# Kernel tuning notes

Measured on AMD Instinct MI355X. Metric: run time of the kernel, lower is better.

Reference implementation:

```python
import jax, jax.numpy as jnp
import numpy as np

N, NUM_TOKENS, TOKEN_DIM = 32768, 8192, 768
K = 4  # hard-coded top-k in the torch forward


def setup_inputs() -> dict:
    key = jax.random.key(0)
    k1, k2 = jax.random.split(key)
    inputs_flatten = jax.random.normal(k1, (N, TOKEN_DIM), dtype=jnp.float32)
    embed = jax.random.normal(k2, (NUM_TOKENS, TOKEN_DIM), dtype=jnp.float32)  # codebook buffer
    return {"inputs_flatten": inputs_flatten, "embed": embed}


def reference(inputs_flatten, embed):
    # squared euclidean distances: [N, num_tokens]
    distances = (
        jnp.sum(inputs_flatten ** 2, axis=1, keepdims=True)
        + jnp.sum(embed ** 2, axis=1)
        - 2.0 * (inputs_flatten @ embed.T)
    )

    # k smallest distances via top_k on negated distances
    neg_vals, topk_indices = jax.lax.top_k(-distances, K)
    topk_values = -neg_vals  # ascending smallest-k distances, [N, 4]

    # drop nearest, reweight the next 3 neighbors
    tv = topk_values[:, 1:]  # [N, 3]
    tv = tv / jnp.maximum(jnp.linalg.norm(tv, axis=1, keepdims=True), 1e-12)  # F.normalize
    tv = 1.0 / (tv + 1e-4)
    topk_values = jax.nn.softmax(tv, axis=1)
    topk_indices_out = topk_indices[:, 1:]

    # hard assignment (argmin) and codebook lookup (one-hot scatter + matmul == gather)
    encoding_indices = jnp.argmin(distances, axis=1)[:, None]  # [N, 1]
    quantize = embed[encoding_indices[:, 0]]  # [N, token_dim]

    # straight-through estimator
    quantize = jax.lax.stop_gradient(quantize - inputs_flatten) + inputs_flatten
    return quantize, encoding_indices, topk_values, topk_indices_out
```

## Files before the change

### kernel.cpp

```cpp
#include <hip/hip_runtime.h>
#include <cfloat>
#include <cmath>

#define NROWS 32768
#define NTOK  8192
#define DIM   768
#define KSPLIT 384

#define BM 64
#define BN 128
#define BK 32
#define NT 512

#define Q_OFF   0
#define EI_OFF  (NROWS*DIM)
#define TV_OFF  (EI_OFF + NROWS)
#define TI_OFF  (TV_OFF + NROWS*3)

typedef short short8 __attribute__((ext_vector_type(8)));
typedef float f32x4 __attribute__((ext_vector_type(4)));
typedef float f32x16 __attribute__((ext_vector_type(16)));

__global__ __launch_bounds__(256)
void np_norm_kernel(const float* __restrict__ x, float* __restrict__ o) {
#pragma clang fp contract(off)
  const int wid = (blockIdx.x * 256 + threadIdx.x) >> 6;
  const int lane = threadIdx.x & 63;
  const float* p = x + (size_t)wid * DIM + (lane >> 3) * 96 + (lane & 7);
  float v = p[0];
  float r = v * v;
#pragma unroll
  for (int k = 1; k < 12; k++) {
    float w = p[8 * k];
    float sq = w * w;
    r = r + sq;
  }
#pragma unroll
  for (int m = 1; m < 64; m <<= 1) {
    float other = __shfl_xor(r, m, 64);
    r = r + other;
  }
  if (lane == 0) o[wid] = r;
}

__device__ __forceinline__ bool dless(float a, int ai, float b, int bi_) {
  return (a < b) || (a == b && ai < bi_);
}

__device__ __forceinline__ void ins4(float (&v)[4], int (&x)[4], float c, int ci) {
  if (dless(c, ci, v[3], x[3])) {
    v[3] = c; x[3] = ci;
    if (dless(v[3], x[3], v[2], x[2])) { float tv = v[2]; int ti = x[2]; v[2] = v[3]; x[2] = x[3]; v[3] = tv; x[3] = ti; }
    if (dless(v[2], x[2], v[1], x[1])) { float tv = v[1]; int ti = x[1]; v[1] = v[2]; x[1] = x[2]; v[2] = tv; x[2] = ti; }
    if (dless(v[1], x[1], v[0], x[0])) { float tv = v[0]; int ti = x[0]; v[0] = v[1]; x[0] = x[1]; v[1] = tv; x[1] = ti; }
  }
}

__device__ __forceinline__ void ins8(float (&v)[8], int (&x)[8], float c, int ci) {
  if (dless(c, ci, v[7], x[7])) {
    v[7] = c; x[7] = ci;
#pragma unroll
    for (int k = 7; k > 0; k--) {
      if (dless(v[k], x[k], v[k - 1], x[k - 1])) {
        float tv = v[k - 1]; int ti = x[k - 1];
        v[k - 1] = v[k]; x[k - 1] = x[k];
        v[k] = tv; x[k] = ti;
      }
    }
  }
}

__device__ __forceinline__ void ins8v(float (&v)[8], int (&x)[8], float c, int ci) {
  v[7] = c; x[7] = ci;
#pragma unroll
  for (int k = 7; k > 0; k--) {
    const bool sw = v[k] < v[k - 1];
    const float vmin = fminf(v[k], v[k - 1]);
    const float vmax = fmaxf(v[k], v[k - 1]);
    const int xk1 = sw ? x[k] : x[k - 1];
    const int xk  = sw ? x[k - 1] : x[k];
    v[k - 1] = vmin; v[k] = vmax;
    x[k - 1] = xk1;  x[k] = xk;
  }
}

__device__ __forceinline__ unsigned short f2bf(float f) {
  unsigned int u = __float_as_uint(f);
  u += 0x7FFFu + ((u >> 16) & 1u);
  return (unsigned short)(u >> 16);
}

typedef const __attribute__((address_space(1))) void* gas1_t;
typedef __attribute__((address_space(3))) void* las3_t;
__device__ __forceinline__ void gl16(const void* g, void* s) {
  __builtin_amdgcn_global_load_lds((gas1_t)g, (las3_t)s, 16, 0, 0);
}

__global__ __launch_bounds__(256)
void cvtT_kernel(const float* __restrict__ in, unsigned short* __restrict__ out, int nrows) {
  __shared__ int4 tile[32][33];
  const int r0 = blockIdx.x * 32;
  const int Q0 = blockIdx.y * 32;
  const int t = threadIdx.x;
#pragma unroll
  for (int i = 0; i < 4; ++i) {
    const int f = t + i * 256;
    const int qi = f & 31, ri = f >> 5;
    const float4* p = (const float4*)(in + (size_t)(r0 + ri) * DIM + (Q0 + qi) * 8);
    const float4 a = p[0], b = p[1];
    union { unsigned short u[8]; int4 v; } pk;
    pk.u[0] = f2bf(a.x); pk.u[1] = f2bf(a.y); pk.u[2] = f2bf(a.z); pk.u[3] = f2bf(a.w);
    pk.u[4] = f2bf(b.x); pk.u[5] = f2bf(b.y); pk.u[6] = f2bf(b.z); pk.u[7] = f2bf(b.w);
    tile[qi][ri] = pk.v;
  }
  __syncthreads();
#pragma unroll
  for (int i = 0; i < 4; ++i) {
    const int f = t + i * 256;
    const int ri = f & 31, qi = f >> 5;
    *(int4*)(out + ((size_t)(Q0 + qi) * nrows + r0 + ri) * 8) = tile[qi][ri];
  }
}

#define STRIPS 16
#define KSTEPS 24
#define NITER (STRIPS * KSTEPS)

__global__ __launch_bounds__(256, 2)
void vq_rank(const unsigned short* __restrict__ xbT, const unsigned short* __restrict__ ebT,
             const float* __restrict__ e2g, unsigned short* __restrict__ topp) {
  __shared__ __align__(16) unsigned char esm[4][16384];

  const int tid = threadIdx.x;
  const int l = tid & 63;
  const int w = tid >> 6;
  const int wr = w >> 1, wc = w & 1;
  const int l31 = l & 31, h = l >> 5;

  const int bid = (int)blockIdx.x;
  const int sbid = (bid & 7) * 64 + (bid >> 3);
  const int chalf = sbid >> 8;
  const int row0 = (sbid & 255) * 128;
  const int cg0 = chalf * 4096;

  const size_t xinv0 = ((size_t)h * NROWS + row0 + wr * 64 + l31) * 8;
  const size_t xinv1 = xinv0 + 32 * 8;

  float bv[2][8]; int bi[2][8];
#pragma unroll
  for (int xj = 0; xj < 2; ++xj)
#pragma unroll
    for (int c = 0; c < 8; ++c) { bv[xj][c] = FLT_MAX; bi[xj][c] = 0x7FFFFFFF; }

  f32x16 acc[4][2];
#pragma unroll
  for (int ei = 0; ei < 4; ++ei)
#pragma unroll
    for (int xj = 0; xj < 2; ++xj) acc[ei][xj] = (f32x16)0.f;

  short8 xb0[4], xb1[4];

#define STAGE_E(BN_, KT, COL0)                                                  \
  {                                                                             \
    const unsigned short* eg = ebT + ((size_t)(4 * (KT)) * NTOK + (COL0) + tid) * 8; \
    gl16(eg,                &esm[BN_][(0 * 256 + w * 64) * 16]);                \
    gl16(eg + NTOK * 8,     &esm[BN_][(1 * 256 + w * 64) * 16]);                \
    gl16(eg + 2 * NTOK * 8, &esm[BN_][(2 * 256 + w * 64) * 16]);                \
    gl16(eg + 3 * NTOK * 8, &esm[BN_][(3 * 256 + w * 64) * 16]);                \
  }

#define XLOAD(XB, KT)                                                           \
  {                                                                             \
    const unsigned short* xp = xbT + (size_t)(4 * (KT)) * (NROWS * 8);          \
    XB[0] = *(const short8*)(xp + xinv0);                                       \
    XB[1] = *(const short8*)(xp + xinv1);                                       \
    XB[2] = *(const short8*)(xp + 2 * NROWS * 8 + xinv0);                       \
    XB[3] = *(const short8*)(xp + 2 * NROWS * 8 + xinv1);                       \
  }

#define SELECT(SC0)                                                             \
  {                                                                             \
    _Pragma("unroll")                                                           \
    for (int ei = 0; ei < 4; ++ei) {                                            \
      const int cb = (SC0) + wc * 128 + ei * 32 + 4 * h;                        \
      float4 e2q[4];                                                            \
      _Pragma("unroll")                                                         \
      for (int q = 0; q < 4; ++q)                                               \
        e2q[q] = *(const float4*)(e2g + cb + q * 8);                            \
      _Pragma("unroll")                                                         \
      for (int xj = 0; xj < 2; ++xj) {                                          \
        _Pragma("unroll")                                                       \
        for (int q = 0; q < 4; ++q) {                                           \
          const float c0 = fmaf(-2.f, acc[ei][xj][q * 4 + 0], e2q[q].x);        \
          const float c1 = fmaf(-2.f, acc[ei][xj][q * 4 + 1], e2q[q].y);        \
          const float c2 = fmaf(-2.f, acc[ei][xj][q * 4 + 2], e2q[q].z);        \
          const float c3 = fmaf(-2.f, acc[ei][xj][q * 4 + 3], e2q[q].w);        \
          if (c0 < bv[xj][7]) ins8v(bv[xj], bi[xj], c0, cb + q * 8 + 0);        \
          if (c1 < bv[xj][7]) ins8v(bv[xj], bi[xj], c1, cb + q * 8 + 1);        \
          if (c2 < bv[xj][7]) ins8v(bv[xj], bi[xj], c2, cb + q * 8 + 2);        \
          if (c3 < bv[xj][7]) ins8v(bv[xj], bi[xj], c3, cb + q * 8 + 3);        \
        }                                                                       \
      }                                                                         \
    }                                                                           \
    _Pragma("unroll")                                                           \
    for (int ei = 0; ei < 4; ++ei)                                              \
      _Pragma("unroll")                                                         \
      for (int xj = 0; xj < 2; ++xj) acc[ei][xj] = (f32x16)0.f;                 \
  }

#define BODY(B_, XB, DO_X, DO_S, WAITS)                                         \
  {                                                                             \
    asm volatile(WAITS ::: "memory");                                           \
    __builtin_amdgcn_s_barrier();                                               \
    asm volatile("" ::: "memory");                                              \
    const unsigned char* ebp = &esm[B_][0];                                     \
    short8 afA[4];                                                              \
    _Pragma("unroll")                                                           \
    for (int ei = 0; ei < 4; ++ei)                                              \
      afA[ei] = *(const short8*)(ebp + (size_t)(h * 256 + wc * 128 + ei * 32 + l31) * 16); \
    if (DO_S) {                                                                 \
      STAGE_E((B_ + 3) & 3, nkt, ncol0)                                         \
      if (++nkt == KSTEPS) { nkt = 0; ncol0 += 256; }                           \
    }                                                                           \
    __builtin_amdgcn_s_barrier();                                               \
    asm volatile("s_waitcnt lgkmcnt(0)" ::: "memory");                          \
    __builtin_amdgcn_sched_barrier(0);                                          \
    __builtin_amdgcn_s_setprio(1);                                              \
    _Pragma("unroll")                                                           \
    for (int ei = 0; ei < 4; ++ei) {                                            \
      acc[ei][0] = __builtin_amdgcn_mfma_f32_32x32x16_bf16(afA[ei], XB[0], acc[ei][0], 0, 0, 0); \
      acc[ei][1] = __builtin_amdgcn_mfma_f32_32x32x16_bf16(afA[ei], XB[1], acc[ei][1], 0, 0, 0); \
    }                                                                           \
    __builtin_amdgcn_s_setprio(0);                                              \
    __builtin_amdgcn_s_barrier();                                               \
    short8 afB[4];                                                              \
    _Pragma("unroll")                                                           \
    for (int ei = 0; ei < 4; ++ei)                                              \
      afB[ei] = *(const short8*)(ebp + (size_t)((2 + h) * 256 + wc * 128 + ei * 32 + l31) * 16); \
    __builtin_amdgcn_s_barrier();                                               \
    asm volatile("s_waitcnt lgkmcnt(0)" ::: "memory");                          \
    __builtin_amdgcn_sched_barrier(0);                                          \
    __builtin_amdgcn_s_setprio(1);                                              \
    _Pragma("unroll")                                                           \
    for (int ei = 0; ei < 4; ++ei) {                                            \
      acc[ei][0] = __builtin_amdgcn_mfma_f32_32x32x16_bf16(afB[ei], XB[2], acc[ei][0], 0, 0, 0); \
      acc[ei][1] = __builtin_amdgcn_mfma_f32_32x32x16_bf16(afB[ei], XB[3], acc[ei][1], 0, 0, 0); \
    }                                                                           \
    __builtin_amdgcn_s_setprio(0);                                              \
    if (DO_X) { XLOAD(XB, xkt) if (++xkt == KSTEPS) xkt = 0; }                  \
    if (++kc == KSTEPS) { SELECT(scol0) kc = 0; scol0 += 256; }                 \
  }

  STAGE_E(0, 0, cg0)
  XLOAD(xb0, 0)
  STAGE_E(1, 1, cg0)
  XLOAD(xb1, 1)
  STAGE_E(2, 2, cg0)

  int xkt = 2;
  int nkt = 3, ncol0 = cg0;
  int kc = 0, scol0 = cg0;

#pragma unroll 1
  for (int g = 0; g < 95; ++g) {
    BODY(0, xb0, 1, 1, "s_waitcnt vmcnt(16)")
    BODY(1, xb1, 1, 1, "s_waitcnt vmcnt(16)")
    BODY(2, xb0, 1, 1, "s_waitcnt vmcnt(16)")
    BODY(3, xb1, 1, 1, "s_waitcnt vmcnt(16)")
  }
  BODY(0, xb0, 1, 1, "s_waitcnt vmcnt(16)")
  BODY(1, xb1, 1, 0, "s_waitcnt vmcnt(12)")
  BODY(2, xb0, 0, 0, "s_waitcnt vmcnt(8)")
  BODY(3, xb1, 0, 0, "s_waitcnt vmcnt(4)")
#undef BODY
#undef SELECT
#undef XLOAD
#undef STAGE_E

#pragma unroll
  for (int xj = 0; xj < 2; ++xj) {
    float ov[8]; int oi[8];
#pragma unroll
    for (int c = 0; c < 8; ++c) {
      ov[c] = __shfl_xor(bv[xj][c], 32, 64);
      oi[c] = __shfl_xor(bi[xj][c], 32, 64);
    }
#pragma unroll
    for (int c = 0; c < 8; ++c) ins8(bv[xj], bi[xj], ov[c], oi[c]);
  }

  __syncthreads();
  float* mval = (float*)&esm[0][0];
  int*   midx = (int*)&esm[1][0];
  if (wc == 1 && l < 32) {
#pragma unroll
    for (int xj = 0; xj < 2; ++xj) {
      const int rr = wr * 64 + xj * 32 + l31;
#pragma unroll
      for (int c = 0; c < 8; ++c) {
        mval[rr * 8 + c] = bv[xj][c];
        midx[rr * 8 + c] = bi[xj][c];
      }
    }
  }
  __syncthreads();
  if (wc == 0 && l < 32) {
#pragma unroll
    for (int xj = 0; xj < 2; ++xj) {
      const int rr = wr * 64 + xj * 32 + l31;
#pragma unroll
      for (int c = 0; c < 8; ++c) ins8(bv[xj], bi[xj], mval[rr * 8 + c], midx[rr * 8 + c]);
      unsigned short* dst = topp + (size_t)(row0 + rr) * 16 + chalf * 8;
#pragma unroll
      for (int c = 0; c < 8; ++c) dst[c] = (unsigned short)bi[xj][c];
    }
  }
}

__global__ __launch_bounds__(256)
void vq_refine16(const float* __restrict__ x, const float* __restrict__ E,
                 const float* __restrict__ x2, const float* __restrict__ e2,
                 const unsigned short* __restrict__ topp, float* __restrict__ out) {
  const int gid = blockIdx.x * 256 + threadIdx.x;
  const int row = gid >> 4;
  const int s = gid & 15;
  const int myc = topp[(size_t)row * 16 + s];

  const float4* xr = (const float4*)(x + (size_t)row * DIM);
  const float4* er = (const float4*)(E + (size_t)myc * DIM);
  float accA = 0.f, accB = 0.f;
#pragma unroll 8
  for (int q = 0; q < KSPLIT / 4; ++q) {
    const float4 a = xr[q], b = er[q];
    accA = fmaf(a.x, b.x, accA); accA = fmaf(a.y, b.y, accA);
    accA = fmaf(a.z, b.z, accA); accA = fmaf(a.w, b.w, accA);
  }
#pragma unroll 8
  for (int q = KSPLIT / 4; q < DIM / 4; ++q) {
    const float4 a = xr[q], b = er[q];
    accB = fmaf(a.x, b.x, accB); accB = fmaf(a.y, b.y, accB);
    accB = fmaf(a.z, b.z, accB); accB = fmaf(a.w, b.w, accB);
  }
  const float d = fmaf(-2.0f, accA + accB, x2[row] + e2[myc]);

  const int base = (threadIdx.x & 63) & ~15;
  float dv[16]; int cv[16];
#pragma unroll
  for (int t = 0; t < 16; ++t) {
    dv[t] = __shfl(d, base + t, 64);
    cv[t] = __shfl(myc, base + t, 64);
  }
#pragma unroll
  for (int a = 0; a < 4; ++a)
#pragma unroll
    for (int b = 15; b > a; --b) {
      const bool sw = (dv[b] < dv[b - 1]) || (dv[b] == dv[b - 1] && cv[b] < cv[b - 1]);
      if (sw) {
        float td = dv[b]; dv[b] = dv[b - 1]; dv[b - 1] = td;
        int ti = cv[b]; cv[b] = cv[b - 1]; cv[b - 1] = ti;
      }
    }

  if (s == 0) {
    out[EI_OFF + row] = (float)cv[0];
    const double d1 = (double)dv[1], d2 = (double)dv[2], d3 = (double)dv[3];
    double nrm = sqrt(d1 * d1 + d2 * d2 + d3 * d3);
    nrm = fmax(nrm, 1e-12);
    const double t1 = 1.0 / (d1 / nrm + 1e-4);
    const double t2 = 1.0 / (d2 / nrm + 1e-4);
    const double t3 = 1.0 / (d3 / nrm + 1e-4);
    const double mx = fmax(t1, fmax(t2, t3));
    const double e1 = exp(t1 - mx), e2x = exp(t2 - mx), e3 = exp(t3 - mx);
    const double sm = e1 + e2x + e3;
    out[TV_OFF + row * 3 + 0] = (float)(e1 / sm);
    out[TV_OFF + row * 3 + 1] = (float)(e2x / sm);
    out[TV_OFF + row * 3 + 2] = (float)(e3 / sm);
    out[TI_OFF + row * 3 + 0] = (float)cv[1];
    out[TI_OFF + row * 3 + 1] = (float)cv[2];
    out[TI_OFF + row * 3 + 2] = (float)cv[3];
  }

  const float4* src = (const float4*)(E + (size_t)cv[0] * DIM);
  float4* dst = (float4*)(out + Q_OFF + (size_t)row * DIM);
#pragma unroll
  for (int k = 0; k < 12; ++k) dst[s + k * 16] = src[s + k * 16];
}

__global__ __launch_bounds__(NT, 4)
void vq_main(const float* __restrict__ A, const float* __restrict__ E,
             const float* __restrict__ x2, const float* __restrict__ e2,
             float* __restrict__ out) {
  __shared__ float a_s[BK][BM + 4];
  __shared__ float b_s[BK][BN + 4];

  const int tid = threadIdx.x;
  const int tx = tid & 15;
  const int ty = tid >> 4;
  const int row0 = blockIdx.x * BM;

  const float x2r[2] = { x2[row0 + ty * 2 + 0], x2[row0 + ty * 2 + 1] };

  float bv[2][4];
  int   bi[2][4];
#pragma unroll
  for (int i = 0; i < 2; i++)
#pragma unroll
    for (int c = 0; c < 4; c++) { bv[i][c] = FLT_MAX; bi[i][c] = 0x7FFFFFFF; }

#define GEMM_STEP(k0, ACC)                                                       \
    {                                                                            \
      __syncthreads();                                                           \
      {                                                                          \
        const int r = tid >> 3, kq = tid & 7;                                    \
        const float4 v = *(const float4*)(A + (size_t)(row0 + r) * DIM + (k0 + kq * 4)); \
        a_s[kq * 4 + 0][r] = v.x; a_s[kq * 4 + 1][r] = v.y;                      \
        a_s[kq * 4 + 2][r] = v.z; a_s[kq * 4 + 3][r] = v.w;                      \
        _Pragma("unroll")                                                        \
        for (int s = 0; s < 2; s++) {                                            \
          const int fi = tid + s * NT;                                           \
          const int rb = fi >> 3, kb = fi & 7;                                   \
          const float4 w = *(const float4*)(E + (size_t)(col0 + rb) * DIM + (k0 + kb * 4)); \
          b_s[kb * 4 + 0][rb] = w.x; b_s[kb * 4 + 1][rb] = w.y;                  \
          b_s[kb * 4 + 2][rb] = w.z; b_s[kb * 4 + 3][rb] = w.w;                  \
        }                                                                        \
      }                                                                          \
      __syncthreads();                                                           \
      _Pragma("unroll")                                                          \
      for (int k = 0; k < BK; k++) {                                             \
        const float2 a2 = *(const float2*)&a_s[k][ty * 2];                       \
        float br[8];                                                             \
        *(float4*)(br)     = *(const float4*)&b_s[k][tx * 8];                    \
        *(float4*)(br + 4) = *(const float4*)&b_s[k][tx * 8 + 4];                \
        _Pragma("unroll")                                                        \
        for (int j = 0; j < 8; j++) {                                            \
          ACC[0][j] = fmaf(a2.x, br[j], ACC[0][j]);                              \
          ACC[1][j] = fmaf(a2.y, br[j], ACC[1][j]);                              \
        }                                                                        \
      }                                                                          \
    }

  for (int ct = 0; ct < NTOK / BN; ++ct) {
    const int col0 = ct * BN;

    float accA[2][8], accB[2][8];
#pragma unroll
    for (int i = 0; i < 2; i++)
#pragma unroll
      for (int j = 0; j < 8; j++) { accA[i][j] = 0.f; accB[i][j] = 0.f; }

    for (int k0 = 0; k0 < KSPLIT; k0 += BK) GEMM_STEP(k0, accA)
    for (int k0 = KSPLIT; k0 < DIM; k0 += BK) GEMM_STEP(k0, accB)

    float e2v[8];
    *(float4*)(e2v)     = *(const float4*)(e2 + col0 + tx * 8);
    *(float4*)(e2v + 4) = *(const float4*)(e2 + col0 + tx * 8 + 4);
#pragma unroll
    for (int i = 0; i < 2; i++) {
#pragma unroll
      for (int j = 0; j < 8; j++) {
        const float dot = accA[i][j] + accB[i][j];
        const float se = x2r[i] + e2v[j];
        const float d = fmaf(-2.0f, dot, se);
        const int ci = col0 + tx * 8 + j;
        ins4(bv[i], bi[i], d, ci);
      }
    }
  }
#undef GEMM_STEP

#pragma unroll
  for (int m = 1; m < 16; m <<= 1) {
#pragma unroll
    for (int i = 0; i < 2; i++) {
      float ov[4]; int oi[4];
#pragma unroll
      for (int c = 0; c < 4; c++) {
        ov[c] = __shfl_xor(bv[i][c], m, 64);
        oi[c] = __shfl_xor(bi[i][c], m, 64);
      }
#pragma unroll
      for (int c = 0; c < 4; c++) ins4(bv[i], bi[i], ov[c], oi[c]);
    }
  }

#pragma unroll
  for (int i = 0; i < 2; i++) {
    if (tx == i) {
      const int gr = row0 + ty * 2 + i;
      out[EI_OFF + gr] = (float)bi[i][0];
      const double d1 = (double)bv[i][1], d2 = (double)bv[i][2], d3 = (double)bv[i][3];
      double nrm = sqrt(d1 * d1 + d2 * d2 + d3 * d3);
      nrm = fmax(nrm, 1e-12);
      const double t1 = 1.0 / (d1 / nrm + 1e-4);
      const double t2 = 1.0 / (d2 / nrm + 1e-4);
      const double t3 = 1.0 / (d3 / nrm + 1e-4);
      const double mx = fmax(t1, fmax(t2, t3));
      const double e1 = exp(t1 - mx), e2x = exp(t2 - mx), e3 = exp(t3 - mx);
      const double s = e1 + e2x + e3;
      out[TV_OFF + gr * 3 + 0] = (float)(e1 / s);
      out[TV_OFF + gr * 3 + 1] = (float)(e2x / s);
      out[TV_OFF + gr * 3 + 2] = (float)(e3 / s);
      out[TI_OFF + gr * 3 + 0] = (float)bi[i][1];
      out[TI_OFF + gr * 3 + 1] = (float)bi[i][2];
      out[TI_OFF + gr * 3 + 2] = (float)bi[i][3];
    }
  }

  __syncthreads();
  int* idx_sh = (int*)&a_s[0][0];
  if (tx == 0) idx_sh[ty * 2 + 0] = bi[0][0];
  if (tx == 1) idx_sh[ty * 2 + 1] = bi[1][0];
  __syncthreads();

  for (int f = tid; f < BM * (DIM / 4); f += NT) {
    const int r = f / (DIM / 4);
    const int c = f % (DIM / 4);
    const int e = idx_sh[r];
    const float4 v = *(const float4*)(E + (size_t)e * DIM + c * 4);
    *(float4*)(out + Q_OFF + (size_t)(row0 + r) * DIM + c * 4) = v;
  }
}

extern "C" void kernel_launch(void* const* d_in, const int* in_sizes, int n_in,
                              void* d_out, int out_size, void* d_ws, size_t ws_size,
                              hipStream_t stream) {
  const float* x = (const float*)d_in[0];
  const float* E = (const float*)d_in[1];
  float* out = (float*)d_out;

  unsigned char* ws = (unsigned char*)d_ws;
  float* e2 = (float*)ws;
  float* x2 = (float*)(ws + 32768);
  unsigned short* topp = (unsigned short*)(ws + 32768 + 131072);
  unsigned short* xbT = (unsigned short*)(ws + 32768 + 131072 + 1048576);
  unsigned short* ebT = xbT + (size_t)NROWS * DIM;
  const size_t need = 32768 + 131072 + 1048576 +
                      (size_t)NROWS * DIM * 2 + (size_t)NTOK * DIM * 2;

  np_norm_kernel<<<NTOK / 4, 256, 0, stream>>>(E, e2);
  np_norm_kernel<<<NROWS / 4, 256, 0, stream>>>(x, x2);

  if (ws_size >= need) {
    cvtT_kernel<<<dim3(NROWS / 32, 3), 256, 0, stream>>>(x, xbT, NROWS);
    cvtT_kernel<<<dim3(NTOK / 32, 3), 256, 0, stream>>>(E, ebT, NTOK);
    vq_rank<<<512, 256, 0, stream>>>(xbT, ebT, e2, topp);
    vq_refine16<<<NROWS * 16 / 256, 256, 0, stream>>>(x, E, x2, e2, topp, out);
  } else {
    vq_main<<<NROWS / BM, NT, 0, stream>>>(x, E, x2, e2, out);
  }
}
```

Before: 929.5 us.

## Restructure vq_rank tiling to one 32-row strip per wave with double-buffered LDS

Each wave now owns a distinct 32-row slab and all 128 codebook columns of a strip, instead of a 2x2 wave grid over 64 rows and 128 columns. LDS staging drops from four buffers to two of 16KB, and launch bounds rise to three blocks per SM. Because waves no longer split columns, the cross-wave LDS merge of top-8 lists disappears. The aims are higher occupancy and a simpler epilogue, at the cost of less reuse of each A fragment, more LDS reads per MFMA, and a shallower prefetch pipeline.

```diff
diff --git a/kernel.cpp b/kernel.cpp
--- a/kernel.cpp
+++ b/kernel.cpp
@@ -75,12 +75,12 @@
 #pragma unroll
   for (int k = 7; k > 0; k--) {
     const bool sw = v[k] < v[k - 1];
-    const float vmin = fminf(v[k], v[k - 1]);
-    const float vmax = fmaxf(v[k], v[k - 1]);
-    const int xk1 = sw ? x[k] : x[k - 1];
-    const int xk  = sw ? x[k - 1] : x[k];
-    v[k - 1] = vmin; v[k] = vmax;
-    x[k - 1] = xk1;  x[k] = xk;
+    const float lo = fminf(v[k], v[k - 1]);
+    const float hi = fmaxf(v[k], v[k - 1]);
+    const int xlo = sw ? x[k] : x[k - 1];
+    const int xhi = sw ? x[k - 1] : x[k];
+    v[k - 1] = lo; v[k] = hi;
+    x[k - 1] = xlo; x[k] = xhi;
   }
 }
 
@@ -122,198 +122,154 @@
   }
 }
 
-#define STRIPS 16
-#define KSTEPS 24
-#define NITER (STRIPS * KSTEPS)
-
-__global__ __launch_bounds__(256, 2)
+__global__ __launch_bounds__(256, 3)
 void vq_rank(const unsigned short* __restrict__ xbT, const unsigned short* __restrict__ ebT,
              const float* __restrict__ e2g, unsigned short* __restrict__ topp) {
-  __shared__ __align__(16) unsigned char esm[4][16384];
+  __shared__ __align__(16) unsigned char esm[2][16384];
 
   const int tid = threadIdx.x;
   const int l = tid & 63;
   const int w = tid >> 6;
-  const int wr = w >> 1, wc = w & 1;
   const int l31 = l & 31, h = l >> 5;
 
   const int bid = (int)blockIdx.x;
   const int sbid = (bid & 7) * 64 + (bid >> 3);
   const int chalf = sbid >> 8;
-  const int row0 = (sbid & 255) * 128;
+  const int rowblk = sbid & 255;
+  const int row0 = rowblk * 128;
   const int cg0 = chalf * 4096;
 
-  const size_t xinv0 = ((size_t)h * NROWS + row0 + wr * 64 + l31) * 8;
-  const size_t xinv1 = xinv0 + 32 * 8;
-
-  float bv[2][8]; int bi[2][8];
-#pragma unroll
-  for (int xj = 0; xj < 2; ++xj)
-#pragma unroll
-    for (int c = 0; c < 8; ++c) { bv[xj][c] = FLT_MAX; bi[xj][c] = 0x7FFFFFFF; }
-
-  f32x16 acc[4][2];
-#pragma unroll
-  for (int ei = 0; ei < 4; ++ei)
-#pragma unroll
-    for (int xj = 0; xj < 2; ++xj) acc[ei][xj] = (f32x16)0.f;
-
-  short8 xb0[4], xb1[4];
-
-#define STAGE_E(BN_, KT, COL0)                                                  \
+  const size_t xinv = ((size_t)h * NROWS + row0 + w * 32 + l31) * 8;
+
+  float bv[8]; int bi[8];
+#pragma unroll
+  for (int c = 0; c < 8; ++c) { bv[c] = FLT_MAX; bi[c] = 0x7FFFFFFF; }
+
+  f32x16 acc[4];
+#pragma unroll
+  for (int ei = 0; ei < 4; ++ei) acc[ei] = (f32x16)0.f;
+
+  short8 xb0[2], xb1[2];
+
+#define STAGE(BN_, KS, STRIP)                                                   \
   {                                                                             \
-    const unsigned short* eg = ebT + ((size_t)(4 * (KT)) * NTOK + (COL0) + tid) * 8; \
-    gl16(eg,                &esm[BN_][(0 * 256 + w * 64) * 16]);                \
-    gl16(eg + NTOK * 8,     &esm[BN_][(1 * 256 + w * 64) * 16]);                \
-    gl16(eg + 2 * NTOK * 8, &esm[BN_][(2 * 256 + w * 64) * 16]);                \
-    gl16(eg + 3 * NTOK * 8, &esm[BN_][(3 * 256 + w * 64) * 16]);                \
+    const int Qb = (KS) * 8 + (tid >> 7);                                       \
+    const int colg = cg0 + (STRIP) * 128 + (tid & 127);                         \
+    _Pragma("unroll")                                                           \
+    for (int c = 0; c < 4; ++c) {                                               \
+      gl16(ebT + ((size_t)(Qb + 2 * c) * NTOK + colg) * 8,                      \
+           &esm[BN_][c * 4096 + tid * 16]);                                     \
+    }                                                                           \
   }
 
 #define XLOAD(XB, KT)                                                           \
   {                                                                             \
     const unsigned short* xp = xbT + (size_t)(4 * (KT)) * (NROWS * 8);          \
-    XB[0] = *(const short8*)(xp + xinv0);                                       \
-    XB[1] = *(const short8*)(xp + xinv1);                                       \
-    XB[2] = *(const short8*)(xp + 2 * NROWS * 8 + xinv0);                       \
-    XB[3] = *(const short8*)(xp + 2 * NROWS * 8 + xinv1);                       \
+    XB[0] = *(const short8*)(xp + xinv);                                        \
+    XB[1] = *(const short8*)(xp + 2 * NROWS * 8 + xinv);                        \
+  }
+
+#define ITER(P, J, XBC, XBN)                                                    \
+  {                                                                             \
+    XLOAD(XBN, xkt) if (++xkt == 24) xkt = 0;                                   \
+    const unsigned char* ebp = &esm[P][0];                                      \
+    short8 af[4];                                                               \
+    _Pragma("unroll")                                                           \
+    for (int ei = 0; ei < 4; ++ei)                                              \
+      af[ei] = *(const short8*)(ebp + (J) * 8192 + h * 2048 + (ei * 32 + l31) * 16); \
+    __builtin_amdgcn_s_setprio(1);                                              \
+    _Pragma("unroll")                                                           \
+    for (int ei = 0; ei < 4; ++ei)                                              \
+      acc[ei] = __builtin_amdgcn_mfma_f32_32x32x16_bf16(af[ei], XBC[0], acc[ei], 0, 0, 0); \
+    __builtin_amdgcn_s_setprio(0);                                              \
+    _Pragma("unroll")                                                           \
+    for (int ei = 0; ei < 4; ++ei)                                              \
+      af[ei] = *(const short8*)(ebp + (J) * 8192 + 4096 + h * 2048 + (ei * 32 + l31) * 16); \
+    __builtin_amdgcn_s_setprio(1);                                              \
+    _Pragma("unroll")                                                           \
+    for (int ei = 0; ei < 4; ++ei)                                              \
+      acc[ei] = __builtin_amdgcn_mfma_f32_32x32x16_bf16(af[ei], XBC[1], acc[ei], 0, 0, 0); \
+    __builtin_amdgcn_s_setprio(0);                                              \
   }
 
 #define SELECT(SC0)                                                             \
   {                                                                             \
     _Pragma("unroll")                                                           \
     for (int ei = 0; ei < 4; ++ei) {                                            \
-      const int cb = (SC0) + wc * 128 + ei * 32 + 4 * h;                        \
+      const int cb = (SC0) + ei * 32 + 4 * h;                                   \
       float4 e2q[4];                                                            \
       _Pragma("unroll")                                                         \
       for (int q = 0; q < 4; ++q)                                               \
         e2q[q] = *(const float4*)(e2g + cb + q * 8);                            \
       _Pragma("unroll")                                                         \
-      for (int xj = 0; xj < 2; ++xj) {                                          \
-        _Pragma("unroll")                                                       \
-        for (int q = 0; q < 4; ++q) {                                           \
-          const float c0 = fmaf(-2.f, acc[ei][xj][q * 4 + 0], e2q[q].x);        \
-          const float c1 = fmaf(-2.f, acc[ei][xj][q * 4 + 1], e2q[q].y);        \
-          const float c2 = fmaf(-2.f, acc[ei][xj][q * 4 + 2], e2q[q].z);        \
-          const float c3 = fmaf(-2.f, acc[ei][xj][q * 4 + 3], e2q[q].w);        \
-          if (c0 < bv[xj][7]) ins8v(bv[xj], bi[xj], c0, cb + q * 8 + 0);        \
-          if (c1 < bv[xj][7]) ins8v(bv[xj], bi[xj], c1, cb + q * 8 + 1);        \
-          if (c2 < bv[xj][7]) ins8v(bv[xj], bi[xj], c2, cb + q * 8 + 2);        \
-          if (c3 < bv[xj][7]) ins8v(bv[xj], bi[xj], c3, cb + q * 8 + 3);        \
-        }                                                                       \
+      for (int q = 0; q < 4; ++q) {                                             \
+        const float c0 = fmaf(-2.f, acc[ei][q * 4 + 0], e2q[q].x);              \
+        const float c1 = fmaf(-2.f, acc[ei][q * 4 + 1], e2q[q].y);              \
+        const float c2 = fmaf(-2.f, acc[ei][q * 4 + 2], e2q[q].z);              \
+        const float c3 = fmaf(-2.f, acc[ei][q * 4 + 3], e2q[q].w);              \
+        if (c0 < bv[7]) ins8v(bv, bi, c0, cb + q * 8 + 0);                      \
+        if (c1 < bv[7]) ins8v(bv, bi, c1, cb + q * 8 + 1);                      \
+        if (c2 < bv[7]) ins8v(bv, bi, c2, cb + q * 8 + 2);                      \
+        if (c3 < bv[7]) ins8v(bv, bi, c3, cb + q * 8 + 3);                      \
       }                                                                         \
     }                                                                           \
     _Pragma("unroll")                                                           \
-    for (int ei = 0; ei < 4; ++ei)                                              \
-      _Pragma("unroll")                                                         \
-      for (int xj = 0; xj < 2; ++xj) acc[ei][xj] = (f32x16)0.f;                 \
-  }
-
-#define BODY(B_, XB, DO_X, DO_S, WAITS)                                         \
+    for (int ei = 0; ei < 4; ++ei) acc[ei] = (f32x16)0.f;                       \
+  }
+
+#define BODY(P, DO_S, WAITS)                                                    \
   {                                                                             \
+    if (DO_S) {                                                                 \
+      STAGE(P ^ 1, nks, nstrip)                                                 \
+      if (++nks == 12) { nks = 0; ++nstrip; }                                   \
+    }                                                                           \
     asm volatile(WAITS ::: "memory");                                           \
     __builtin_amdgcn_s_barrier();                                               \
     asm volatile("" ::: "memory");                                              \
-    const unsigned char* ebp = &esm[B_][0];                                     \
-    short8 afA[4];                                                              \
-    _Pragma("unroll")                                                           \
-    for (int ei = 0; ei < 4; ++ei)                                              \
-      afA[ei] = *(const short8*)(ebp + (size_t)(h * 256 + wc * 128 + ei * 32 + l31) * 16); \
-    if (DO_S) {                                                                 \
-      STAGE_E((B_ + 3) & 3, nkt, ncol0)                                         \
-      if (++nkt == KSTEPS) { nkt = 0; ncol0 += 256; }                           \
-    }                                                                           \
+    ITER(P, 0, xb0, xb1)                                                        \
+    ITER(P, 1, xb1, xb0)                                                        \
+    if (++kc == 12) { SELECT(scol0) kc = 0; scol0 += 128; }                     \
     __builtin_amdgcn_s_barrier();                                               \
-    asm volatile("s_waitcnt lgkmcnt(0)" ::: "memory");                          \
-    __builtin_amdgcn_sched_barrier(0);                                          \
-    __builtin_amdgcn_s_setprio(1);                                              \
-    _Pragma("unroll")                                                           \
-    for (int ei = 0; ei < 4; ++ei) {                                            \
-      acc[ei][0] = __builtin_amdgcn_mfma_f32_32x32x16_bf16(afA[ei], XB[0], acc[ei][0], 0, 0, 0); \
-      acc[ei][1] = __builtin_amdgcn_mfma_f32_32x32x16_bf16(afA[ei], XB[1], acc[ei][1], 0, 0, 0); \
-    }                                                                           \
-    __builtin_amdgcn_s_setprio(0);                                              \
-    __builtin_amdgcn_s_barrier();                                               \
-    short8 afB[4];                                                              \
-    _Pragma("unroll")                                                           \
-    for (int ei = 0; ei < 4; ++ei)                                              \
-      afB[ei] = *(const short8*)(ebp + (size_t)((2 + h) * 256 + wc * 128 + ei * 32 + l31) * 16); \
-    __builtin_amdgcn_s_barrier();                                               \
-    asm volatile("s_waitcnt lgkmcnt(0)" ::: "memory");                          \
-    __builtin_amdgcn_sched_barrier(0);                                          \
-    __builtin_amdgcn_s_setprio(1);                                              \
-    _Pragma("unroll")                                                           \
-    for (int ei = 0; ei < 4; ++ei) {                                            \
-      acc[ei][0] = __builtin_amdgcn_mfma_f32_32x32x16_bf16(afB[ei], XB[2], acc[ei][0], 0, 0, 0); \
-      acc[ei][1] = __builtin_amdgcn_mfma_f32_32x32x16_bf16(afB[ei], XB[3], acc[ei][1], 0, 0, 0); \
-    }                                                                           \
-    __builtin_amdgcn_s_setprio(0);                                              \
-    if (DO_X) { XLOAD(XB, xkt) if (++xkt == KSTEPS) xkt = 0; }                  \
-    if (++kc == KSTEPS) { SELECT(scol0) kc = 0; scol0 += 256; }                 \
-  }
-
-  STAGE_E(0, 0, cg0)
+  }
+
+  STAGE(0, 0, 0)
   XLOAD(xb0, 0)
-  STAGE_E(1, 1, cg0)
-  XLOAD(xb1, 1)
-  STAGE_E(2, 2, cg0)
-
-  int xkt = 2;
-  int nkt = 3, ncol0 = cg0;
+  asm volatile("s_waitcnt vmcnt(0)" ::: "memory");
+  __builtin_amdgcn_s_barrier();
+
+  int nks = 1, nstrip = 0;
+  int xkt = 1;
   int kc = 0, scol0 = cg0;
 
 #pragma unroll 1
-  for (int g = 0; g < 95; ++g) {
-    BODY(0, xb0, 1, 1, "s_waitcnt vmcnt(16)")
-    BODY(1, xb1, 1, 1, "s_waitcnt vmcnt(16)")
-    BODY(2, xb0, 1, 1, "s_waitcnt vmcnt(16)")
-    BODY(3, xb1, 1, 1, "s_waitcnt vmcnt(16)")
-  }
-  BODY(0, xb0, 1, 1, "s_waitcnt vmcnt(16)")
-  BODY(1, xb1, 1, 0, "s_waitcnt vmcnt(12)")
-  BODY(2, xb0, 0, 0, "s_waitcnt vmcnt(8)")
-  BODY(3, xb1, 0, 0, "s_waitcnt vmcnt(4)")
+  for (int gp = 0; gp < 191; ++gp) {
+    BODY(0, 1, "s_waitcnt vmcnt(8)")
+    BODY(1, 1, "s_waitcnt vmcnt(8)")
+  }
+  BODY(0, 1, "s_waitcnt vmcnt(8)")
+  BODY(1, 0, "s_waitcnt vmcnt(4)")
 #undef BODY
 #undef SELECT
+#undef ITER
 #undef XLOAD
-#undef STAGE_E
-
-#pragma unroll
-  for (int xj = 0; xj < 2; ++xj) {
+#undef STAGE
+
+  {
     float ov[8]; int oi[8];
 #pragma unroll
     for (int c = 0; c < 8; ++c) {
-      ov[c] = __shfl_xor(bv[xj][c], 32, 64);
-      oi[c] = __shfl_xor(bi[xj][c], 32, 64);
-    }
-#pragma unroll
-    for (int c = 0; c < 8; ++c) ins8(bv[xj], bi[xj], ov[c], oi[c]);
-  }
-
-  __syncthreads();
-  float* mval = (float*)&esm[0][0];
-  int*   midx = (int*)&esm[1][0];
-  if (wc == 1 && l < 32) {
-#pragma unroll
-    for (int xj = 0; xj < 2; ++xj) {
-      const int rr = wr * 64 + xj * 32 + l31;
-#pragma unroll
-      for (int c = 0; c < 8; ++c) {
-        mval[rr * 8 + c] = bv[xj][c];
-        midx[rr * 8 + c] = bi[xj][c];
-      }
-    }
-  }
-  __syncthreads();
-  if (wc == 0 && l < 32) {
-#pragma unroll
-    for (int xj = 0; xj < 2; ++xj) {
-      const int rr = wr * 64 + xj * 32 + l31;
-#pragma unroll
-      for (int c = 0; c < 8; ++c) ins8(bv[xj], bi[xj], mval[rr * 8 + c], midx[rr * 8 + c]);
-      unsigned short* dst = topp + (size_t)(row0 + rr) * 16 + chalf * 8;
-#pragma unroll
-      for (int c = 0; c < 8; ++c) dst[c] = (unsigned short)bi[xj][c];
-    }
+      ov[c] = __shfl_xor(bv[c], 32, 64);
+      oi[c] = __shfl_xor(bi[c], 32, 64);
+    }
+#pragma unroll
+    for (int c = 0; c < 8; ++c) ins8(bv, bi, ov[c], oi[c]);
+  }
+
+  if (l < 32) {
+    const int row = row0 + w * 32 + l31;
+    unsigned short* dst = topp + (size_t)row * 16 + chalf * 8;
+#pragma unroll
+    for (int c = 0; c < 8; ++c) dst[c] = (unsigned short)bi[c];
   }
 }
 
```

After: 1.429 ms. +53.7%, slower.
